# Kernel optimization log

Hardware: AMD Instinct MI355X
Metric: run time of the kernel (lower is better)

The kernel has to match this reference:

```python
import jax, jax.numpy as jnp
import numpy as np

N_CELL, N_TISSUE, H, NH = 200000, 2000, 256, 8
HD = H // NH
SCALE = HD ** -0.5
EPS = 1e-5


def _layernorm(x, g, b):
    m = jnp.mean(x, axis=-1, keepdims=True)
    v = jnp.mean((x - m) ** 2, axis=-1, keepdims=True)
    return (x - m) / jnp.sqrt(v + EPS) * g + b


def setup_inputs() -> dict:
    key = jax.random.key(0)
    ks = jax.random.split(key, 12)
    s = 0.02

    def lin(k):
        k1, k2 = jax.random.split(k)
        return (jax.random.normal(k1, (H, H), jnp.float32) * s,
                jax.random.normal(k2, (H,), jnp.float32) * s)

    Wq_bu, bq_bu = lin(ks[0])
    Wk_bu, bk_bu = lin(ks[1])
    Wv_bu, bv_bu = lin(ks[2])
    Wo_bu, bo_bu = lin(ks[3])
    Wv_td, bv_td = lin(ks[4])
    Wo_td, bo_td = lin(ks[5])
    return dict(
        cell_features=jax.random.normal(ks[6], (N_CELL, H), jnp.float32),
        tissue_features=jax.random.normal(ks[7], (N_TISSUE, H), jnp.float32),
        cluster_labels=jax.random.randint(ks[8], (N_CELL,), 0, N_TISSUE, dtype=jnp.int32),
        tissue_batch=jnp.zeros((N_TISSUE,), jnp.int32),
        Wq_bu=Wq_bu, bq_bu=bq_bu, Wk_bu=Wk_bu, bk_bu=bk_bu,
        Wv_bu=Wv_bu, bv_bu=bv_bu, Wo_bu=Wo_bu, bo_bu=bo_bu,
        Wv_td=Wv_td, bv_td=bv_td, Wo_td=Wo_td, bo_td=bo_td,
        ln_cell_g=jnp.ones((H,), jnp.float32), ln_cell_b=jnp.zeros((H,), jnp.float32),
        ln_tissue_g=jnp.ones((H,), jnp.float32), ln_tissue_b=jnp.zeros((H,), jnp.float32),
    )


def reference(cell_features, tissue_features, cluster_labels, tissue_batch,
              Wq_bu, bq_bu, Wk_bu, bk_bu, Wv_bu, bv_bu, Wo_bu, bo_bu,
              Wv_td, bv_td, Wo_td, bo_td,
              ln_cell_g, ln_cell_b, ln_tissue_g, ln_tissue_b):
    Nc = cell_features.shape[0]
    Nt = tissue_features.shape[0]

    # ---- bottom-up: each tissue node (1 query) attends over its cells (segment attention) ----
    Q = (tissue_features @ Wq_bu + bq_bu).reshape(Nt, NH, HD)   # [Nt, h, d]
    K = (cell_features @ Wk_bu + bk_bu).reshape(Nc, NH, HD)     # [Nc, h, d]
    V = (cell_features @ Wv_bu + bv_bu).reshape(Nc, NH, HD)     # [Nc, h, d]

    # per-cell score against its own cluster's tissue query
    scores = jnp.einsum('nhd,nhd->nh', K, Q[cluster_labels]) * SCALE  # [Nc, h]
    smax = jax.lax.stop_gradient(
        jax.ops.segment_max(scores, cluster_labels, num_segments=Nt))  # [Nt, h]
    ex = jnp.exp(scores - smax[cluster_labels])
    denom = jax.ops.segment_sum(ex, cluster_labels, num_segments=Nt)   # [Nt, h]
    w = ex / denom[cluster_labels]                                     # [Nc, h]
    attended = jax.ops.segment_sum(w[..., None] * V, cluster_labels,
                                   num_segments=Nt)                    # [Nt, h, d]
    attended = attended.reshape(Nt, H) @ Wo_bu + bo_bu

    counts = jax.ops.segment_sum(jnp.ones((Nc,), cell_features.dtype),
                                 cluster_labels, num_segments=Nt)
    tissue_updated = jnp.where(counts[:, None] > 0, attended, tissue_features)

    # ---- top-down: each cell attends to its single tissue token ----
    # softmax over a single key is identically 1, so q/k projections cancel:
    # attended_cell = out_proj(v_proj(tissue_updated[cluster]))
    td_per_tissue = (tissue_updated @ Wv_td + bv_td) @ Wo_td + bo_td   # [Nt, H]
    cell_updated = td_per_tissue[cluster_labels]                       # [Nc, H]

    cell_out = _layernorm(cell_features + cell_updated, ln_cell_g, ln_cell_b)
    tissue_out = _layernorm(tissue_features + tissue_updated, ln_tissue_g, ln_tissue_b)
    return (cell_out, tissue_out)
```

## Files before the change

### kernel.cpp

```cpp
#include <hip/hip_runtime.h>
#include <math.h>

#define NC 200000
#define NT 2000
#define HH 256
#define NH_ 8
#define SCALE 0.17677669529663687f
#define EPS 1e-5f
#define SMAX 1024


__global__ void k_hist(const int* __restrict__ labels, int* __restrict__ counts) {
  int i = blockIdx.x * 256 + threadIdx.x;
  if (i < NC) atomicAdd(&counts[labels[i]], 1);
}

__global__ void k_scan(const int* __restrict__ counts, int* __restrict__ offsets) {
  int tid = threadIdx.x;
  int base = tid * 32;
  int local[32];
  int s = 0;
  #pragma unroll
  for (int k = 0; k < 32; k++) {
    int idx = base + k;
    int v = (idx < NT) ? counts[idx] : 0;
    local[k] = s;
    s += v;
  }
  int incl = s;
  #pragma unroll
  for (int d = 1; d < 64; d <<= 1) {
    int o = __shfl_up(incl, d, 64);
    if (tid >= d) incl += o;
  }
  int excl = incl - s;
  #pragma unroll
  for (int k = 0; k < 32; k++) {
    int idx = base + k;
    if (idx < NT) offsets[idx] = excl + local[k];
  }
  if (tid == 63) offsets[NT] = incl;
}

__global__ void k_scatter(const int* __restrict__ labels, const int* __restrict__ offsets,
                          int* __restrict__ cursor, int* __restrict__ cindex) {
  int i = blockIdx.x * 256 + threadIdx.x;
  if (i < NC) {
    int c = labels[i];
    int pos = offsets[c] + atomicAdd(&cursor[c], 1);
    cindex[pos] = i;
  }
}


__global__ __launch_bounds__(256) void k_gemm_bias(
    const float* __restrict__ A, const float* __restrict__ W,
    const float* __restrict__ bias, float* __restrict__ C, int M)
{
  __shared__ float Al[16][33];
  __shared__ float Wl[32][HH];
  int tid = threadIdx.x;
  int r0 = blockIdx.x * 16;
  float acc[16];
  #pragma unroll
  for (int r = 0; r < 16; r++) acc[r] = 0.f;
  for (int k0 = 0; k0 < HH; k0 += 32) {
    for (int e = tid; e < 16 * 32; e += 256) {
      int r = e >> 5, k = e & 31;
      int row = r0 + r;
      Al[r][k] = (row < M) ? A[(size_t)row * HH + k0 + k] : 0.f;
    }
    for (int e = tid; e < 32 * HH; e += 256) {
      int k = e >> 8, j = e & 255;
      Wl[k][j] = W[(size_t)(k0 + k) * HH + j];
    }
    __syncthreads();
    for (int k = 0; k < 32; k++) {
      float w = Wl[k][tid];
      #pragma unroll
      for (int r = 0; r < 16; r++) acc[r] += Al[r][k] * w;
    }
    __syncthreads();
  }
  float bj = bias[tid];
  #pragma unroll
  for (int r = 0; r < 16; r++) {
    int row = r0 + r;
    if (row < M) C[(size_t)row * HH + tid] = acc[r] + bj;
  }
}


__global__ __launch_bounds__(256) void k_qproj(
    const float* __restrict__ Q, const float* __restrict__ Wk, float* __restrict__ Qproj)
{
  __shared__ float Al[64][33];
  __shared__ float Bl[32][257];
  int h = blockIdx.x & 7, tb = blockIdx.x >> 3;
  int t0 = tb * 64;
  int tid = threadIdx.x;
  for (int e = tid; e < 64 * 32; e += 256) {
    int r = e >> 5, d = e & 31;
    int t = t0 + r;
    Al[r][d] = (t < NT) ? Q[(size_t)t * HH + h * 32 + d] * SCALE : 0.f;
  }
  for (int e = tid; e < 256 * 32; e += 256) {
    int j = e >> 5, d = e & 31;
    Bl[d][j] = Wk[(size_t)j * HH + h * 32 + d];
  }
  __syncthreads();
  float acc[64];
  #pragma unroll
  for (int r = 0; r < 64; r++) acc[r] = 0.f;
  for (int d = 0; d < 32; d++) {
    float b = Bl[d][tid];
    #pragma unroll
    for (int r = 0; r < 64; r++) acc[r] += Al[r][d] * b;
  }
  for (int r = 0; r < 64; r++) {
    int t = t0 + r;
    if (t < NT) Qproj[((size_t)t * NH_ + h) * HH + tid] = acc[r];
  }
}

__global__ void k_bkq(const float* __restrict__ Q, const float* __restrict__ bk,
                      float* __restrict__ bkq) {
  int g = blockIdx.x * 256 + threadIdx.x;
  if (g < NT * NH_) {
    int t = g >> 3, h = g & 7;
    float s = 0.f;
    #pragma unroll
    for (int d = 0; d < 32; d++) s += bk[h * 32 + d] * Q[(size_t)t * HH + h * 32 + d];
    bkq[g] = s * SCALE;
  }
}


__device__ inline unsigned pk2(float a, float b) {
  unsigned ua = (__float_as_uint(a) + 0x8000u) >> 16;
  unsigned ub = (__float_as_uint(b) + 0x8000u) & 0xFFFF0000u;
  return ua | ub;
}
__device__ inline void unpk8(uint4 v, float* s) {
  s[0] = __uint_as_float(v.x << 16); s[1] = __uint_as_float(v.x & 0xFFFF0000u);
  s[2] = __uint_as_float(v.y << 16); s[3] = __uint_as_float(v.y & 0xFFFF0000u);
  s[4] = __uint_as_float(v.z << 16); s[5] = __uint_as_float(v.z & 0xFFFF0000u);
  s[6] = __uint_as_float(v.w << 16); s[7] = __uint_as_float(v.w & 0xFFFF0000u);
}


__global__ __launch_bounds__(256) void k_cellpass2(
    const float* __restrict__ cell, const int* __restrict__ cindex,
    const int* __restrict__ offsets, const float* __restrict__ Qproj,
    const float* __restrict__ bkq, float* __restrict__ Cwn)
{
  __shared__ float qp_lds[NH_][HH];
  __shared__ uint4 slds[SMAX];
  __shared__ float cwlds[NH_][HH];
  __shared__ float red[4][NH_];

  int t = blockIdx.x;
  int n0 = offsets[t], n1 = offsets[t + 1];
  int ncells = n1 - n0;
  if (ncells <= 0) return;
  if (ncells > SMAX) ncells = SMAX;
  int tid = threadIdx.x;
  int w = tid >> 6, lane = tid & 63;
  int slot = lane >> 3, g = lane & 7;

  for (int e = tid; e < NH_ * HH / 4; e += 256)
    ((float4*)qp_lds)[e] = ((const float4*)(Qproj + (size_t)t * NH_ * HH))[e];
  float bq[NH_];
  #pragma unroll
  for (int h = 0; h < NH_; h++) bq[h] = bkq[t * NH_ + h];
  __syncthreads();

  float m[NH_];
  #pragma unroll
  for (int h = 0; h < NH_; h++) m[h] = -1e30f;

  int nsweep = (ncells + 15) >> 4;
  for (int j = w; j < nsweep; j += 4) {
    int base = n0 + j * 16;
    int ia = base + slot, ib = base + 8 + slot;
    int na = cindex[min(ia, n1 - 1)];
    int nb = cindex[min(ib, n1 - 1)];
    float4 xa[8], xb[8];
    #pragma unroll
    for (int k = 0; k < 8; k++)
      xa[k] = *reinterpret_cast<const float4*>(&cell[(size_t)na * HH + g * 4 + 32 * k]);
    #pragma unroll
    for (int k = 0; k < 8; k++)
      xb[k] = *reinterpret_cast<const float4*>(&cell[(size_t)nb * HH + g * 4 + 32 * k]);

    float pa[NH_], pb[NH_];
    #pragma unroll
    for (int h = 0; h < NH_; h++) { pa[h] = 0.f; pb[h] = 0.f; }
    #pragma unroll
    for (int h = 0; h < NH_; h++) {
      #pragma unroll
      for (int k = 0; k < 8; k++) {
        float4 q = *reinterpret_cast<const float4*>(&qp_lds[h][g * 4 + 32 * k]);
        pa[h] += xa[k].x * q.x + xa[k].y * q.y + xa[k].z * q.z + xa[k].w * q.w;
        pb[h] += xb[k].x * q.x + xb[k].y * q.y + xb[k].z * q.z + xb[k].w * q.w;
      }
    }
    #pragma unroll
    for (int d = 1; d < 8; d <<= 1) {
      #pragma unroll
      for (int h = 0; h < NH_; h++) {
        pa[h] += __shfl_xor(pa[h], d, 64);
        pb[h] += __shfl_xor(pb[h], d, 64);
      }
    }
    #pragma unroll
    for (int h = 0; h < NH_; h++) { pa[h] += bq[h]; pb[h] += bq[h]; }
    bool va = ia < n1, vb = ib < n1;
    if (va) {
      #pragma unroll
      for (int h = 0; h < NH_; h++) m[h] = fmaxf(m[h], pa[h]);
    }
    if (vb) {
      #pragma unroll
      for (int h = 0; h < NH_; h++) m[h] = fmaxf(m[h], pb[h]);
    }
    if (g == 0) {
      if (va) slds[ia - n0] = make_uint4(pk2(pa[0], pa[1]), pk2(pa[2], pa[3]),
                                         pk2(pa[4], pa[5]), pk2(pa[6], pa[7]));
      if (vb) slds[ib - n0] = make_uint4(pk2(pb[0], pb[1]), pk2(pb[2], pb[3]),
                                         pk2(pb[4], pb[5]), pk2(pb[6], pb[7]));
    }
  }

  #pragma unroll
  for (int d = 8; d < 64; d <<= 1) {
    #pragma unroll
    for (int h = 0; h < NH_; h++) m[h] = fmaxf(m[h], __shfl_xor(m[h], d, 64));
  }
  if (lane == 0) {
    #pragma unroll
    for (int h = 0; h < NH_; h++) red[w][h] = m[h];
  }
  __syncthreads();
  #pragma unroll
  for (int h = 0; h < NH_; h++)
    m[h] = fmaxf(fmaxf(red[0][h], red[1][h]), fmaxf(red[2][h], red[3][h]));
  __syncthreads();

  float dsum[NH_];
  #pragma unroll
  for (int h = 0; h < NH_; h++) dsum[h] = 0.f;
  for (int i = tid; i < ncells; i += 256) {
    uint4 sv = slds[i];
    float s[NH_], e[NH_];
    unpk8(sv, s);
    #pragma unroll
    for (int h = 0; h < NH_; h++) { e[h] = __expf(s[h] - m[h]); dsum[h] += e[h]; }
    slds[i] = make_uint4(pk2(e[0], e[1]), pk2(e[2], e[3]), pk2(e[4], e[5]), pk2(e[6], e[7]));
  }
  #pragma unroll
  for (int d = 1; d < 64; d <<= 1) {
    #pragma unroll
    for (int h = 0; h < NH_; h++) dsum[h] += __shfl_xor(dsum[h], d, 64);
  }
  if (lane == 0) {
    #pragma unroll
    for (int h = 0; h < NH_; h++) red[w][h] = dsum[h];
  }
  __syncthreads();
  float dinv[NH_];
  #pragma unroll
  for (int h = 0; h < NH_; h++)
    dinv[h] = 1.f / (red[0][h] + red[1][h] + red[2][h] + red[3][h]);

  float cw[NH_][4];
  #pragma unroll
  for (int h = 0; h < NH_; h++) { cw[h][0] = cw[h][1] = cw[h][2] = cw[h][3] = 0.f; }
  for (int i = w; i < ncells; i += 4) {
    int n = cindex[n0 + i];
    float4 x = *reinterpret_cast<const float4*>(&cell[(size_t)n * HH + lane * 4]);
    float e[NH_];
    unpk8(slds[i], e);
    #pragma unroll
    for (int h = 0; h < NH_; h++) {
      cw[h][0] += e[h] * x.x; cw[h][1] += e[h] * x.y;
      cw[h][2] += e[h] * x.z; cw[h][3] += e[h] * x.w;
    }
  }
  if (w == 0) {
    #pragma unroll
    for (int h = 0; h < NH_; h++)
      *reinterpret_cast<float4*>(&cwlds[h][lane * 4]) =
          make_float4(cw[h][0], cw[h][1], cw[h][2], cw[h][3]);
  }
  __syncthreads();
  #pragma unroll
  for (int ww = 1; ww < 4; ww++) {
    if (w == ww) {
      #pragma unroll
      for (int h = 0; h < NH_; h++) {
        float4 c = *reinterpret_cast<float4*>(&cwlds[h][lane * 4]);
        c.x += cw[h][0]; c.y += cw[h][1]; c.z += cw[h][2]; c.w += cw[h][3];
        *reinterpret_cast<float4*>(&cwlds[h][lane * 4]) = c;
      }
    }
    __syncthreads();
  }
  #pragma unroll
  for (int h = 0; h < NH_; h++)
    Cwn[((size_t)t * NH_ + h) * HH + tid] = cwlds[h][tid] * dinv[h];
}


#define TCH 8

__global__ __launch_bounds__(256) void k_tissuechain(
    const float* __restrict__ tissue, const int* __restrict__ counts,
    const float* __restrict__ Cwn,
    const float* __restrict__ Wv, const float* __restrict__ bv,
    const float* __restrict__ Wo, const float* __restrict__ bo,
    const float* __restrict__ Wvtd, const float* __restrict__ bvtd,
    const float* __restrict__ Wotd, const float* __restrict__ botd,
    const float* __restrict__ lng, const float* __restrict__ lnb,
    float* __restrict__ td, float* __restrict__ out_tissue)
{
  __shared__ float s_cwn[TCH][NH_ * HH];
  __shared__ float s_a[TCH][HH];
  __shared__ float s_tu[TCH][HH];
  __shared__ float s_tmp[TCH][HH];
  __shared__ float s_red[2][4];
  int t0 = blockIdx.x * TCH;
  int j = threadIdx.x;
  int h = j >> 5;

  for (int e = j; e < TCH * NH_ * HH; e += 256)
    ((float*)s_cwn)[e] = Cwn[(size_t)t0 * NH_ * HH + e];
  __syncthreads();

  float acc[TCH];
  #pragma unroll
  for (int t = 0; t < TCH; t++) acc[t] = 0.f;
  for (int k = 0; k < HH; k++) {
    float w = Wv[(size_t)k * HH + j];
    #pragma unroll
    for (int t = 0; t < TCH; t++) acc[t] += s_cwn[t][h * HH + k] * w;
  }
  {
    float bj = bv[j];
    #pragma unroll
    for (int t = 0; t < TCH; t++) s_a[t][j] = acc[t] + bj;
  }
  __syncthreads();

  #pragma unroll
  for (int t = 0; t < TCH; t++) acc[t] = 0.f;
  for (int k = 0; k < HH; k++) {
    float w = Wo[(size_t)k * HH + j];
    #pragma unroll
    for (int t = 0; t < TCH; t++) acc[t] += s_a[t][k] * w;
  }
  {
    float bj = bo[j];
    #pragma unroll
    for (int t = 0; t < TCH; t++) {
      int tt = t0 + t;
      s_tu[t][j] = (counts[tt] > 0) ? (acc[t] + bj) : tissue[(size_t)tt * HH + j];
    }
  }
  __syncthreads();

  #pragma unroll
  for (int t = 0; t < TCH; t++) acc[t] = 0.f;
  for (int k = 0; k < HH; k++) {
    float w = Wvtd[(size_t)k * HH + j];
    #pragma unroll
    for (int t = 0; t < TCH; t++) acc[t] += s_tu[t][k] * w;
  }
  {
    float bj = bvtd[j];
    #pragma unroll
    for (int t = 0; t < TCH; t++) s_tmp[t][j] = acc[t] + bj;
  }
  __syncthreads();

  #pragma unroll
  for (int t = 0; t < TCH; t++) acc[t] = 0.f;
  for (int k = 0; k < HH; k++) {
    float w = Wotd[(size_t)k * HH + j];
    #pragma unroll
    for (int t = 0; t < TCH; t++) acc[t] += s_tmp[t][k] * w;
  }
  {
    float bj = botd[j];
    #pragma unroll
    for (int t = 0; t < TCH; t++) td[(size_t)(t0 + t) * HH + j] = acc[t] + bj;
  }

  float gj = lng[j], bj2 = lnb[j];
  for (int t = 0; t < TCH; t++) {
    float y = tissue[(size_t)(t0 + t) * HH + j] + s_tu[t][j];
    float s1 = y, s2 = y * y;
    #pragma unroll
    for (int d = 1; d < 64; d <<= 1) { s1 += __shfl_xor(s1, d, 64); s2 += __shfl_xor(s2, d, 64); }
    int wv_ = j >> 6, ln_ = j & 63;
    __syncthreads();
    if (ln_ == 0) { s_red[0][wv_] = s1; s_red[1][wv_] = s2; }
    __syncthreads();
    s1 = s_red[0][0] + s_red[0][1] + s_red[0][2] + s_red[0][3];
    s2 = s_red[1][0] + s_red[1][1] + s_red[1][2] + s_red[1][3];
    float mean = s1 * (1.f / 256.f);
    float var = s2 * (1.f / 256.f) - mean * mean;
    float inv = rsqrtf(var + EPS);
    out_tissue[(size_t)(t0 + t) * HH + j] = (y - mean) * inv * gj + bj2;
  }
}


__global__ __launch_bounds__(256) void k_cellout(
    const float* __restrict__ cell, const float* __restrict__ td,
    const int* __restrict__ labels,
    const float* __restrict__ lng, const float* __restrict__ lnb,
    float* __restrict__ out)
{
  int row = blockIdx.x * 4 + (threadIdx.x >> 6);
  if (row >= NC) return;
  int lane = threadIdx.x & 63;
  int c = labels[row];
  float4 x = *reinterpret_cast<const float4*>(&cell[(size_t)row * HH + lane * 4]);
  float4 u = *reinterpret_cast<const float4*>(&td[(size_t)c * HH + lane * 4]);
  float y0 = x.x + u.x, y1 = x.y + u.y, y2 = x.z + u.z, y3 = x.w + u.w;
  float s1 = y0 + y1 + y2 + y3;
  float s2 = y0 * y0 + y1 * y1 + y2 * y2 + y3 * y3;
  #pragma unroll
  for (int d = 1; d < 64; d <<= 1) { s1 += __shfl_xor(s1, d, 64); s2 += __shfl_xor(s2, d, 64); }
  float mean = s1 * (1.f / 256.f);
  float var = s2 * (1.f / 256.f) - mean * mean;
  float inv = rsqrtf(var + EPS);
  float4 g = *reinterpret_cast<const float4*>(&lng[lane * 4]);
  float4 b = *reinterpret_cast<const float4*>(&lnb[lane * 4]);
  float4 o;
  o.x = (y0 - mean) * inv * g.x + b.x;
  o.y = (y1 - mean) * inv * g.y + b.y;
  o.z = (y2 - mean) * inv * g.z + b.z;
  o.w = (y3 - mean) * inv * g.w + b.w;
  *reinterpret_cast<float4*>(&out[(size_t)row * HH + lane * 4]) = o;
}


extern "C" void kernel_launch(void* const* d_in, const int* in_sizes, int n_in,
                              void* d_out, int out_size, void* d_ws, size_t ws_size,
                              hipStream_t stream) {
  const float* cell   = (const float*)d_in[0];
  const float* tissue = (const float*)d_in[1];
  const int*   labels = (const int*)d_in[2];
  const float* Wq = (const float*)d_in[4];  const float* bq = (const float*)d_in[5];
  const float* Wk = (const float*)d_in[6];  const float* bk = (const float*)d_in[7];
  const float* Wv = (const float*)d_in[8];  const float* bv = (const float*)d_in[9];
  const float* Wo = (const float*)d_in[10]; const float* bo = (const float*)d_in[11];
  const float* Wvtd = (const float*)d_in[12]; const float* bvtd = (const float*)d_in[13];
  const float* Wotd = (const float*)d_in[14]; const float* botd = (const float*)d_in[15];
  const float* lncg = (const float*)d_in[16]; const float* lncb = (const float*)d_in[17];
  const float* lntg = (const float*)d_in[18]; const float* lntb = (const float*)d_in[19];
  float* out_cell   = (float*)d_out;
  float* out_tissue = (float*)d_out + (size_t)NC * HH;

  char* w = (char*)d_ws;
  auto take = [&](size_t bytes) { void* p = (void*)w; w += (bytes + 255) & ~(size_t)255; return p; };
  int*   counts  = (int*)take((size_t)NT * 4);
  int*   cursor  = (int*)take((size_t)NT * 4);
  int*   offsets = (int*)take((size_t)(NT + 1) * 4);
  int*   cindex  = (int*)take((size_t)NC * 4);
  float* Q       = (float*)take((size_t)NT * HH * 4);
  float* Qproj   = (float*)take((size_t)NT * NH_ * HH * 4);
  float* bkq     = (float*)take((size_t)NT * NH_ * 4);
  float* Cwn     = (float*)take((size_t)NT * NH_ * HH * 4);
  float* td      = (float*)take((size_t)NT * HH * 4);

  hipMemsetAsync(counts, 0, 16384, stream);

  const int CB = (NC + 255) / 256;
  k_hist<<<CB, 256, 0, stream>>>(labels, counts);
  k_scan<<<1, 64, 0, stream>>>(counts, offsets);
  k_scatter<<<CB, 256, 0, stream>>>(labels, offsets, cursor, cindex);

  k_gemm_bias<<<(NT + 15) / 16, 256, 0, stream>>>(tissue, Wq, bq, Q, NT);
  k_qproj<<<8 * ((NT + 63) / 64), 256, 0, stream>>>(Q, Wk, Qproj);
  k_bkq<<<(NT * NH_ + 255) / 256, 256, 0, stream>>>(Q, bk, bkq);

  k_cellpass2<<<NT, 256, 0, stream>>>(cell, cindex, offsets, Qproj, bkq, Cwn);

  k_tissuechain<<<NT / TCH, 256, 0, stream>>>(tissue, counts, Cwn,
      Wv, bv, Wo, bo, Wvtd, bvtd, Wotd, botd, lntg, lntb, td, out_tissue);

  k_cellout<<<NC / 4, 256, 0, stream>>>(cell, td, labels, lncg, lncb, out_cell);
}
```

Measured before the change: 487.6 us.

## Split per-tissue cell pass into fixed-size slices with a separate reduction

```diff
diff --git a/kernel.cpp b/kernel.cpp
--- a/kernel.cpp
+++ b/kernel.cpp
@@ -7,7 +7,9 @@
 #define NH_ 8
 #define SCALE 0.17677669529663687f
 #define EPS 1e-5f
-#define SMAX 1024
+#define SLICE 128
+#define PSLICES (NT + NC / SLICE + 1)
+#define PSTRIDE 2056
 
 
 __global__ void k_hist(const int* __restrict__ labels, int* __restrict__ counts) {
@@ -15,31 +17,41 @@
   if (i < NC) atomicAdd(&counts[labels[i]], 1);
 }
 
-__global__ void k_scan(const int* __restrict__ counts, int* __restrict__ offsets) {
+__global__ void k_scan(const int* __restrict__ counts, int* __restrict__ offsets,
+                       int* __restrict__ soff) {
   int tid = threadIdx.x;
   int base = tid * 32;
-  int local[32];
-  int s = 0;
+  int la[32], lb[32];
+  int sa = 0, sb = 0;
   #pragma unroll
   for (int k = 0; k < 32; k++) {
     int idx = base + k;
     int v = (idx < NT) ? counts[idx] : 0;
-    local[k] = s;
-    s += v;
-  }
-  int incl = s;
+    la[k] = sa; lb[k] = sb;
+    sa += v; sb += (v + SLICE - 1) / SLICE;
+  }
+  int ia_ = sa, ib_ = sb;
   #pragma unroll
   for (int d = 1; d < 64; d <<= 1) {
-    int o = __shfl_up(incl, d, 64);
-    if (tid >= d) incl += o;
-  }
-  int excl = incl - s;
+    int oa = __shfl_up(ia_, d, 64);
+    int ob = __shfl_up(ib_, d, 64);
+    if (tid >= d) { ia_ += oa; ib_ += ob; }
+  }
+  int ea = ia_ - sa, eb = ib_ - sb;
   #pragma unroll
   for (int k = 0; k < 32; k++) {
     int idx = base + k;
-    if (idx < NT) offsets[idx] = excl + local[k];
-  }
-  if (tid == 63) offsets[NT] = incl;
+    if (idx < NT) { offsets[idx] = ea + la[k]; soff[idx] = eb + lb[k]; }
+  }
+  if (tid == 63) { offsets[NT] = ia_; soff[NT] = ib_; }
+}
+
+__global__ void k_slicemap(const int* __restrict__ soff, int* __restrict__ slice_t) {
+  int t = blockIdx.x * 256 + threadIdx.x;
+  if (t < NT) {
+    int s0 = soff[t], s1 = soff[t + 1];
+    for (int s = s0; s < s1; s++) slice_t[s] = t;
+  }
 }
 
 __global__ void k_scatter(const int* __restrict__ labels, const int* __restrict__ offsets,
@@ -136,55 +148,42 @@
 }
 
 
-__device__ inline unsigned pk2(float a, float b) {
-  unsigned ua = (__float_as_uint(a) + 0x8000u) >> 16;
-  unsigned ub = (__float_as_uint(b) + 0x8000u) & 0xFFFF0000u;
-  return ua | ub;
-}
-__device__ inline void unpk8(uint4 v, float* s) {
-  s[0] = __uint_as_float(v.x << 16); s[1] = __uint_as_float(v.x & 0xFFFF0000u);
-  s[2] = __uint_as_float(v.y << 16); s[3] = __uint_as_float(v.y & 0xFFFF0000u);
-  s[4] = __uint_as_float(v.z << 16); s[5] = __uint_as_float(v.z & 0xFFFF0000u);
-  s[6] = __uint_as_float(v.w << 16); s[7] = __uint_as_float(v.w & 0xFFFF0000u);
-}
-
-
-__global__ __launch_bounds__(256) void k_cellpass2(
+__global__ __launch_bounds__(256) void k_cellslice(
     const float* __restrict__ cell, const int* __restrict__ cindex,
-    const int* __restrict__ offsets, const float* __restrict__ Qproj,
-    const float* __restrict__ bkq, float* __restrict__ Cwn)
+    const int* __restrict__ offsets, const int* __restrict__ soff,
+    const int* __restrict__ slice_t,
+    const float* __restrict__ Qproj, const float* __restrict__ bkq,
+    float* __restrict__ Pbuf)
 {
-  __shared__ float qp_lds[NH_][HH];
-  __shared__ uint4 slds[SMAX];
+  __shared__ float qp[NH_][HH];
+  __shared__ float e_lds[SLICE][NH_];
   __shared__ float cwlds[NH_][HH];
   __shared__ float red[4][NH_];
 
-  int t = blockIdx.x;
-  int n0 = offsets[t], n1 = offsets[t + 1];
-  int ncells = n1 - n0;
-  if (ncells <= 0) return;
-  if (ncells > SMAX) ncells = SMAX;
+  int s = blockIdx.x;
+  if (s >= soff[NT]) return;
+  int t = slice_t[s];
+  int l = s - soff[t];
+  int c0 = offsets[t] + l * SLICE;
+  int c1 = min(c0 + SLICE, offsets[t + 1]);
+  int nc = c1 - c0;
+
   int tid = threadIdx.x;
-  int w = tid >> 6, lane = tid & 63;
-  int slot = lane >> 3, g = lane & 7;
+  int w = tid >> 6, lane = tid & 63, slot = lane >> 3, g = lane & 7;
 
   for (int e = tid; e < NH_ * HH / 4; e += 256)
-    ((float4*)qp_lds)[e] = ((const float4*)(Qproj + (size_t)t * NH_ * HH))[e];
+    ((float4*)qp)[e] = ((const float4*)(Qproj + (size_t)t * NH_ * HH))[e];
   float bq[NH_];
   #pragma unroll
   for (int h = 0; h < NH_; h++) bq[h] = bkq[t * NH_ + h];
   __syncthreads();
 
-  float m[NH_];
-  #pragma unroll
-  for (int h = 0; h < NH_; h++) m[h] = -1e30f;
-
-  int nsweep = (ncells + 15) >> 4;
+  int nsweep = (nc + 15) >> 4;
   for (int j = w; j < nsweep; j += 4) {
-    int base = n0 + j * 16;
-    int ia = base + slot, ib = base + 8 + slot;
-    int na = cindex[min(ia, n1 - 1)];
-    int nb = cindex[min(ib, n1 - 1)];
+    int bb = c0 + j * 16;
+    int ia = bb + slot, ib = bb + 8 + slot;
+    int na = cindex[min(ia, c1 - 1)];
+    int nb = cindex[min(ib, c1 - 1)];
     float4 xa[8], xb[8];
     #pragma unroll
     for (int k = 0; k < 8; k++)
@@ -200,7 +199,7 @@
     for (int h = 0; h < NH_; h++) {
       #pragma unroll
       for (int k = 0; k < 8; k++) {
-        float4 q = *reinterpret_cast<const float4*>(&qp_lds[h][g * 4 + 32 * k]);
+        float4 q = *reinterpret_cast<const float4*>(&qp[h][g * 4 + 32 * k]);
         pa[h] += xa[k].x * q.x + xa[k].y * q.y + xa[k].z * q.z + xa[k].w * q.w;
         pb[h] += xb[k].x * q.x + xb[k].y * q.y + xb[k].z * q.z + xb[k].w * q.w;
       }
@@ -213,79 +212,51 @@
         pb[h] += __shfl_xor(pb[h], d, 64);
       }
     }
-    #pragma unroll
-    for (int h = 0; h < NH_; h++) { pa[h] += bq[h]; pb[h] += bq[h]; }
-    bool va = ia < n1, vb = ib < n1;
-    if (va) {
-      #pragma unroll
-      for (int h = 0; h < NH_; h++) m[h] = fmaxf(m[h], pa[h]);
-    }
-    if (vb) {
-      #pragma unroll
-      for (int h = 0; h < NH_; h++) m[h] = fmaxf(m[h], pb[h]);
+    float ea[NH_], eb[NH_];
+    #pragma unroll
+    for (int h = 0; h < NH_; h++) {
+      ea[h] = __expf(pa[h] + bq[h]);
+      eb[h] = __expf(pb[h] + bq[h]);
     }
     if (g == 0) {
-      if (va) slds[ia - n0] = make_uint4(pk2(pa[0], pa[1]), pk2(pa[2], pa[3]),
-                                         pk2(pa[4], pa[5]), pk2(pa[6], pa[7]));
-      if (vb) slds[ib - n0] = make_uint4(pk2(pb[0], pb[1]), pk2(pb[2], pb[3]),
-                                         pk2(pb[4], pb[5]), pk2(pb[6], pb[7]));
-    }
-  }
-
-  #pragma unroll
-  for (int d = 8; d < 64; d <<= 1) {
-    #pragma unroll
-    for (int h = 0; h < NH_; h++) m[h] = fmaxf(m[h], __shfl_xor(m[h], d, 64));
+      if (ia < c1) {
+        *reinterpret_cast<float4*>(&e_lds[ia - c0][0]) = make_float4(ea[0], ea[1], ea[2], ea[3]);
+        *reinterpret_cast<float4*>(&e_lds[ia - c0][4]) = make_float4(ea[4], ea[5], ea[6], ea[7]);
+      }
+      if (ib < c1) {
+        *reinterpret_cast<float4*>(&e_lds[ib - c0][0]) = make_float4(eb[0], eb[1], eb[2], eb[3]);
+        *reinterpret_cast<float4*>(&e_lds[ib - c0][4]) = make_float4(eb[4], eb[5], eb[6], eb[7]);
+      }
+    }
+  }
+  __syncthreads();
+
+  float cw[NH_][4];
+  float dsum[NH_];
+  #pragma unroll
+  for (int h = 0; h < NH_; h++) {
+    cw[h][0] = cw[h][1] = cw[h][2] = cw[h][3] = 0.f;
+    dsum[h] = 0.f;
+  }
+  for (int i = w; i < nc; i += 4) {
+    int n = cindex[c0 + i];
+    float4 x = *reinterpret_cast<const float4*>(&cell[(size_t)n * HH + lane * 4]);
+    float4 e0 = *reinterpret_cast<float4*>(&e_lds[i][0]);
+    float4 e1 = *reinterpret_cast<float4*>(&e_lds[i][4]);
+    cw[0][0] += e0.x * x.x; cw[0][1] += e0.x * x.y; cw[0][2] += e0.x * x.z; cw[0][3] += e0.x * x.w;
+    cw[1][0] += e0.y * x.x; cw[1][1] += e0.y * x.y; cw[1][2] += e0.y * x.z; cw[1][3] += e0.y * x.w;
+    cw[2][0] += e0.z * x.x; cw[2][1] += e0.z * x.y; cw[2][2] += e0.z * x.z; cw[2][3] += e0.z * x.w;
+    cw[3][0] += e0.w * x.x; cw[3][1] += e0.w * x.y; cw[3][2] += e0.w * x.z; cw[3][3] += e0.w * x.w;
+    cw[4][0] += e1.x * x.x; cw[4][1] += e1.x * x.y; cw[4][2] += e1.x * x.z; cw[4][3] += e1.x * x.w;
+    cw[5][0] += e1.y * x.x; cw[5][1] += e1.y * x.y; cw[5][2] += e1.y * x.z; cw[5][3] += e1.y * x.w;
+    cw[6][0] += e1.z * x.x; cw[6][1] += e1.z * x.y; cw[6][2] += e1.z * x.z; cw[6][3] += e1.z * x.w;
+    cw[7][0] += e1.w * x.x; cw[7][1] += e1.w * x.y; cw[7][2] += e1.w * x.z; cw[7][3] += e1.w * x.w;
+    dsum[0] += e0.x; dsum[1] += e0.y; dsum[2] += e0.z; dsum[3] += e0.w;
+    dsum[4] += e1.x; dsum[5] += e1.y; dsum[6] += e1.z; dsum[7] += e1.w;
   }
   if (lane == 0) {
     #pragma unroll
-    for (int h = 0; h < NH_; h++) red[w][h] = m[h];
-  }
-  __syncthreads();
-  #pragma unroll
-  for (int h = 0; h < NH_; h++)
-    m[h] = fmaxf(fmaxf(red[0][h], red[1][h]), fmaxf(red[2][h], red[3][h]));
-  __syncthreads();
-
-  float dsum[NH_];
-  #pragma unroll
-  for (int h = 0; h < NH_; h++) dsum[h] = 0.f;
-  for (int i = tid; i < ncells; i += 256) {
-    uint4 sv = slds[i];
-    float s[NH_], e[NH_];
-    unpk8(sv, s);
-    #pragma unroll
-    for (int h = 0; h < NH_; h++) { e[h] = __expf(s[h] - m[h]); dsum[h] += e[h]; }
-    slds[i] = make_uint4(pk2(e[0], e[1]), pk2(e[2], e[3]), pk2(e[4], e[5]), pk2(e[6], e[7]));
-  }
-  #pragma unroll
-  for (int d = 1; d < 64; d <<= 1) {
-    #pragma unroll
-    for (int h = 0; h < NH_; h++) dsum[h] += __shfl_xor(dsum[h], d, 64);
-  }
-  if (lane == 0) {
-    #pragma unroll
     for (int h = 0; h < NH_; h++) red[w][h] = dsum[h];
-  }
-  __syncthreads();
-  float dinv[NH_];
-  #pragma unroll
-  for (int h = 0; h < NH_; h++)
-    dinv[h] = 1.f / (red[0][h] + red[1][h] + red[2][h] + red[3][h]);
-
-  float cw[NH_][4];
-  #pragma unroll
-  for (int h = 0; h < NH_; h++) { cw[h][0] = cw[h][1] = cw[h][2] = cw[h][3] = 0.f; }
-  for (int i = w; i < ncells; i += 4) {
-    int n = cindex[n0 + i];
-    float4 x = *reinterpret_cast<const float4*>(&cell[(size_t)n * HH + lane * 4]);
-    float e[NH_];
-    unpk8(slds[i], e);
-    #pragma unroll
-    for (int h = 0; h < NH_; h++) {
-      cw[h][0] += e[h] * x.x; cw[h][1] += e[h] * x.y;
-      cw[h][2] += e[h] * x.z; cw[h][3] += e[h] * x.w;
-    }
   }
   if (w == 0) {
     #pragma unroll
@@ -306,9 +277,36 @@
     }
     __syncthreads();
   }
-  #pragma unroll
-  for (int h = 0; h < NH_; h++)
-    Cwn[((size_t)t * NH_ + h) * HH + tid] = cwlds[h][tid] * dinv[h];
+
+  float* pb = Pbuf + (size_t)s * PSTRIDE;
+  #pragma unroll
+  for (int h = 0; h < NH_; h++) pb[h * HH + tid] = cwlds[h][tid];
+  if (tid < NH_) pb[2048 + tid] = red[0][tid] + red[1][tid] + red[2][tid] + red[3][tid];
+}
+
+
+__global__ __launch_bounds__(256) void k_reduce(
+    const float* __restrict__ Pbuf, const int* __restrict__ soff, float* __restrict__ Cwn)
+{
+  int t = blockIdx.x;
+  int s0 = soff[t], ns = soff[t + 1] - s0;
+  int tid = threadIdx.x;
+  #pragma unroll
+  for (int r = 0; r < 2; r++) {
+    int c4 = tid + r * 256;
+    int h = c4 >> 6;
+    float4 acc = make_float4(0.f, 0.f, 0.f, 0.f);
+    float d = 0.f;
+    for (int q = 0; q < ns; q++) {
+      const float* p = Pbuf + (size_t)(s0 + q) * PSTRIDE;
+      float4 v = *reinterpret_cast<const float4*>(&p[c4 * 4]);
+      acc.x += v.x; acc.y += v.y; acc.z += v.z; acc.w += v.w;
+      d += p[2048 + h];
+    }
+    float inv = (ns > 0) ? 1.f / d : 0.f;
+    float4 o = make_float4(acc.x * inv, acc.y * inv, acc.z * inv, acc.w * inv);
+    *reinterpret_cast<float4*>(&Cwn[(size_t)t * 2048 + c4 * 4]) = o;
+  }
 }
 
 
@@ -469,25 +467,31 @@
   int*   counts  = (int*)take((size_t)NT * 4);
   int*   cursor  = (int*)take((size_t)NT * 4);
   int*   offsets = (int*)take((size_t)(NT + 1) * 4);
+  int*   soff    = (int*)take((size_t)(NT + 1) * 4);
+  int*   slice_t = (int*)take((size_t)PSLICES * 4);
   int*   cindex  = (int*)take((size_t)NC * 4);
   float* Q       = (float*)take((size_t)NT * HH * 4);
   float* Qproj   = (float*)take((size_t)NT * NH_ * HH * 4);
   float* bkq     = (float*)take((size_t)NT * NH_ * 4);
   float* Cwn     = (float*)take((size_t)NT * NH_ * HH * 4);
   float* td      = (float*)take((size_t)NT * HH * 4);
+  float* Pbuf    = (float*)take((size_t)PSLICES * PSTRIDE * 4);
 
   hipMemsetAsync(counts, 0, 16384, stream);
 
   const int CB = (NC + 255) / 256;
   k_hist<<<CB, 256, 0, stream>>>(labels, counts);
-  k_scan<<<1, 64, 0, stream>>>(counts, offsets);
+  k_scan<<<1, 64, 0, stream>>>(counts, offsets, soff);
+  k_slicemap<<<(NT + 255) / 256, 256, 0, stream>>>(soff, slice_t);
   k_scatter<<<CB, 256, 0, stream>>>(labels, offsets, cursor, cindex);
 
   k_gemm_bias<<<(NT + 15) / 16, 256, 0, stream>>>(tissue, Wq, bq, Q, NT);
   k_qproj<<<8 * ((NT + 63) / 64), 256, 0, stream>>>(Q, Wk, Qproj);
   k_bkq<<<(NT * NH_ + 255) / 256, 256, 0, stream>>>(Q, bk, bkq);
 
-  k_cellpass2<<<NT, 256, 0, stream>>>(cell, cindex, offsets, Qproj, bkq, Cwn);
+  k_cellslice<<<PSLICES, 256, 0, stream>>>(cell, cindex, offsets, soff, slice_t,
+                                           Qproj, bkq, Pbuf);
+  k_reduce<<<NT, 256, 0, stream>>>(Pbuf, soff, Cwn);
 
   k_tissuechain<<<NT / TCH, 256, 0, stream>>>(tissue, counts, Cwn,
       Wv, bv, Wo, bo, Wvtd, bvtd, Wotd, botd, lntg, lntb, td, out_tissue);
```

Result: no change. 489.2 us (+0.3%).
